# Performance work log

Hardware: AMD Instinct MI355X
Metric: run time of the kernel (lower is better)

## Reference

```python
import jax, jax.numpy as jnp
import numpy as np

B, T, C, H = 4, 1024, 768, 12
HD = C // H  # 64
EPS = 1e-5

def setup_inputs() -> dict:
    key = jax.random.key(0)
    ks = jax.random.split(key, 6)
    s = 0.02
    return {
        "x": jax.random.normal(ks[0], (B, T, C), jnp.float32),
        "ln1_w": jnp.ones((C,), jnp.float32),
        "w_attn": jax.random.normal(ks[1], (C, 3 * C), jnp.float32) * s,
        "w_pos": jax.random.normal(ks[2], (C, C), jnp.float32) * s,
        "w_cproj": jax.random.normal(ks[3], (C, C), jnp.float32) * s,
        "ln2_w": jnp.ones((C,), jnp.float32),
        "w_fc": jax.random.normal(ks[4], (C, 4 * C), jnp.float32) * s,
        "w_mproj": jax.random.normal(ks[5], (4 * C, C), jnp.float32) * s,
    }

def _layernorm(x, w):
    m = jnp.mean(x, axis=-1, keepdims=True)
    v = jnp.mean(jnp.square(x - m), axis=-1, keepdims=True)
    return (x - m) * jax.lax.rsqrt(v + EPS) * w

def _rpe_table(dtype):
    # sinusoidal table over relative distances [-(T-1), T-1] -> [2T-1, HD]
    inv_freq = 1.0 / (10000.0 ** (jnp.arange(0, HD, 2, dtype=jnp.float32) / HD))
    dist = jnp.arange(-(T - 1), T, dtype=jnp.float32)
    freqs = dist[:, None] * inv_freq[None, :]
    return jnp.concatenate([jnp.sin(freqs), jnp.cos(freqs)], axis=-1).astype(dtype)

def reference(x, ln1_w, w_attn, w_pos, w_cproj, ln2_w, w_fc, w_mproj):
    # ---- attention branch ----
    h = _layernorm(x, ln1_w)
    qkv = h @ w_attn                                 # [B,T,3C]
    q, k, v = jnp.split(qkv, 3, axis=-1)
    q = q.reshape(B, T, H, HD).transpose(0, 2, 1, 3)  # [B,H,T,HD]
    k = k.reshape(B, T, H, HD).transpose(0, 2, 1, 3)
    v = v.reshape(B, T, H, HD).transpose(0, 2, 1, 3)
    # note: the original also computes p = c_pos(x) but never uses it (dead code)

    # relative position embeddings gathered to [T,T,HD]
    idx = jnp.arange(T)
    rel = jnp.clip(idx[:, None] - idx[None, :], -(T - 1), T - 1) + (T - 1)
    rpe = _rpe_table(q.dtype)[rel]                    # [T,T,HD]

    scale = 1.0 / np.sqrt(HD)
    att = (jnp.einsum('bhid,bhjd->bhij', q, k)
           + jnp.einsum('bhid,ijd->bhij', q, rpe)) * scale
    causal = idx[:, None] >= idx[None, :]             # [T,T] lower-tri
    att = jnp.where(causal, att, -jnp.inf)
    att = jax.nn.softmax(att, axis=-1)
    y = jnp.einsum('bhij,bhjd->bhid', att, v)         # [B,H,T,HD]
    y = y.transpose(0, 2, 1, 3).reshape(B, T, C) @ w_cproj
    x = x + y

    # ---- MLP branch ----
    h2 = _layernorm(x, ln2_w)
    m = jax.nn.gelu(h2 @ w_fc, approximate=False) @ w_mproj
    return x + m
```

## Files before the change

kernel.cpp:

```cpp
#include <hip/hip_runtime.h>
#include <math.h>

typedef __attribute__((ext_vector_type(8))) short bf16x8;
typedef __attribute__((ext_vector_type(4))) float f32x4;
typedef __attribute__((ext_vector_type(16))) float f32x16;
typedef __attribute__((ext_vector_type(4))) unsigned u32x4;

__device__ inline short f2bf(float f) {
  unsigned u = __builtin_bit_cast(unsigned, f);
  u = u + 0x7fffu + ((u >> 16) & 1u);
  return (short)(u >> 16);
}
__device__ inline float bf2f(short s) {
  return __builtin_bit_cast(float, ((unsigned)(unsigned short)s) << 16);
}

__device__ inline void gload16(const short* g, short* l) {
  __builtin_amdgcn_global_load_lds(
      (const __attribute__((address_space(1))) unsigned*)g,
      (__attribute__((address_space(3))) unsigned*)l, 16, 0, 0);
}

__global__ __launch_bounds__(256) void wtrans_kernel(
    const float* __restrict__ in, short* __restrict__ out, int K, int N) {
  __shared__ float tile[32][33];
  const int tx = threadIdx.x & 31, ty = threadIdx.x >> 5;
  const int n0 = blockIdx.x * 32, k0 = blockIdx.y * 32;
  #pragma unroll
  for (int r = ty; r < 32; r += 8)
    tile[r][tx] = in[(size_t)(k0 + r) * N + n0 + tx];
  __syncthreads();
  #pragma unroll
  for (int r = ty; r < 32; r += 8)
    out[(size_t)(n0 + r) * K + k0 + tx] = f2bf(tile[tx][r]);
}

__global__ __launch_bounds__(256) void ktab_kernel(short* __restrict__ ktab) {
  const int idx = blockIdx.x * 256 + threadIdx.x;
  const int j = idx >> 5, cc = idx & 31;
  const float invf = exp2f(-(float)cc * (13.287712379549449f / 32.0f));
  const float ang = (float)j * invf;
  ktab[j * 64 + cc]      = f2bf(cosf(ang));
  ktab[j * 64 + 32 + cc] = f2bf(sinf(ang));
}

__global__ __launch_bounds__(256) void qprime_kernel(
    const short* __restrict__ qkv, short* __restrict__ qpr) {
  const int idx = blockIdx.x * 256 + threadIdx.x;
  const int cc = idx & 31;
  const int row = idx >> 5;
  const int i = row & 1023, bh = row >> 10;
  const int b = bh / 12, h = bh % 12;
  const float invf = exp2f(-(float)cc * (13.287712379549449f / 32.0f));
  const float ang = (float)i * invf;
  const float si = sinf(ang), co = cosf(ang);
  const short* q = qkv + (size_t)(b * 1024 + i) * 2304 + h * 64;
  const float qs = bf2f(q[cc]), qc = bf2f(q[32 + cc]);
  qpr[(size_t)row * 64 + cc]      = f2bf(qs * si + qc * co);
  qpr[(size_t)row * 64 + 32 + cc] = f2bf(qc * si - qs * co);
}

__global__ __launch_bounds__(256) void ln_kernel(
    const float* __restrict__ x, const float* __restrict__ w,
    short* __restrict__ out) {
  const int row = blockIdx.x, tid = threadIdx.x;
  const float* xr = x + (size_t)row * 768;
  float v0 = xr[tid], v1 = xr[tid + 256], v2 = xr[tid + 512];
  float s = v0 + v1 + v2;
  #pragma unroll
  for (int o = 1; o < 64; o <<= 1) s += __shfl_xor(s, o);
  __shared__ float red[8];
  const int wv = tid >> 6;
  if ((tid & 63) == 0) red[wv] = s;
  __syncthreads();
  const float mean = (red[0] + red[1] + red[2] + red[3]) * (1.0f / 768.0f);
  v0 -= mean; v1 -= mean; v2 -= mean;
  float q = v0 * v0 + v1 * v1 + v2 * v2;
  #pragma unroll
  for (int o = 1; o < 64; o <<= 1) q += __shfl_xor(q, o);
  if ((tid & 63) == 0) red[4 + wv] = q;
  __syncthreads();
  const float var = (red[4] + red[5] + red[6] + red[7]) * (1.0f / 768.0f);
  const float inv = 1.0f / sqrtf(var + 1e-5f);
  out[(size_t)row * 768 + tid]       = f2bf(v0 * inv * w[tid]);
  out[(size_t)row * 768 + tid + 256] = f2bf(v1 * inv * w[tid + 256]);
  out[(size_t)row * 768 + tid + 512] = f2bf(v2 * inv * w[tid + 512]);
}

__global__ __launch_bounds__(256) void vtrans_kernel(
    const short* __restrict__ qkv, short* __restrict__ vT) {
  __shared__ short tile[64][65];
  const int blk = blockIdx.x;
  const int bh = blk >> 4, t0 = (blk & 15) * 64;
  const int b = bh / 12, h = bh % 12;
  const int tx = threadIdx.x & 63, ty = threadIdx.x >> 6;
  const short* src = qkv + (size_t)(b * 1024 + t0) * 2304 + 1536 + h * 64;
  #pragma unroll
  for (int r = ty; r < 64; r += 4)
    tile[r][tx] = src[(size_t)r * 2304 + tx];
  __syncthreads();
  short* dst = vT + (size_t)bh * 64 * 1024 + t0;
  #pragma unroll
  for (int r = ty; r < 64; r += 4)
    dst[(size_t)r * 1024 + tx] = tile[tx][r];
}

template <int EPI, int BM, int BN>
__global__ __launch_bounds__(256) void gemm_bt(
    const short* __restrict__ A, const short* __restrict__ Bt,
    const float* __restrict__ res, float* __restrict__ outF,
    short* __restrict__ outB, int M, int N, int K, int lda, int ldb) {
  __shared__ __align__(16) short As[2][BM * 32];
  __shared__ __align__(16) short Bs[2][BN * 32];
  constexpr int WM = BM / 2, WN = BN / 2;
  constexpr int MI = WM / 16, NJ = WN / 16;
  const int tid = threadIdx.x;
  const int w = tid >> 6, lane = tid & 63;
  const int m0 = blockIdx.y * BM, n0 = blockIdx.x * BN;
  const int wm = (w >> 1) * WM, wn = (w & 1) * WN;
  const int lr = lane >> 2;
  const int lc = (lane & 3) * 8;
  if constexpr (EPI == 3) {
    A += (size_t)blockIdx.z * K;
    Bt += (size_t)blockIdx.z * K;
    outF += (size_t)blockIdx.z * M * N;
  }
  f32x4 acc[MI][NJ];
  #pragma unroll
  for (int i = 0; i < MI; i++)
    #pragma unroll
    for (int j = 0; j < NJ; j++)
      #pragma unroll
      for (int r = 0; r < 4; r++) acc[i][j][r] = 0.0f;

  const int nt = K / 32;
  #pragma unroll
  for (int p = 0; p < BM / 64; ++p)
    gload16(A + (size_t)(m0 + p * 64 + w * 16 + lr) * lda + lc,
            &As[0][p * 2048 + w * 512]);
  #pragma unroll
  for (int p = 0; p < BN / 64; ++p)
    gload16(Bt + (size_t)(n0 + p * 64 + w * 16 + lr) * ldb + lc,
            &Bs[0][p * 2048 + w * 512]);
  __syncthreads();

  for (int t = 0; t < nt; ++t) {
    const int cur = t & 1;
    if (t + 1 < nt) {
      const int kt = (t + 1) * 32;
      #pragma unroll
      for (int p = 0; p < BM / 64; ++p)
        gload16(A + (size_t)(m0 + p * 64 + w * 16 + lr) * lda + kt + lc,
                &As[cur ^ 1][p * 2048 + w * 512]);
      #pragma unroll
      for (int p = 0; p < BN / 64; ++p)
        gload16(Bt + (size_t)(n0 + p * 64 + w * 16 + lr) * ldb + kt + lc,
                &Bs[cur ^ 1][p * 2048 + w * 512]);
    }
    bf16x8 af[MI], bfr[NJ];
    #pragma unroll
    for (int i = 0; i < MI; i++)
      af[i] = *(const bf16x8*)&As[cur][(wm + i * 16 + (lane & 15)) * 32 + (lane >> 4) * 8];
    #pragma unroll
    for (int j = 0; j < NJ; j++)
      bfr[j] = *(const bf16x8*)&Bs[cur][(wn + j * 16 + (lane & 15)) * 32 + (lane >> 4) * 8];
    #pragma unroll
    for (int i = 0; i < MI; i++)
      #pragma unroll
      for (int j = 0; j < NJ; j++)
        acc[i][j] = __builtin_amdgcn_mfma_f32_16x16x32_bf16(af[i], bfr[j],
                                                            acc[i][j], 0, 0, 0);
    __syncthreads();
  }
  const int r0 = (lane >> 4) * 4, cl = lane & 15;
  #pragma unroll
  for (int i = 0; i < MI; i++) {
    #pragma unroll
    for (int j = 0; j < NJ; j++) {
      const int gm = m0 + wm + i * 16 + r0;
      const int gn = n0 + wn + j * 16 + cl;
      #pragma unroll
      for (int r = 0; r < 4; r++) {
        const size_t idx = (size_t)(gm + r) * N + gn;
        const float v = acc[i][j][r];
        if constexpr (EPI == 0) {
          outB[idx] = f2bf(v);
        } else if constexpr (EPI == 1) {
          outF[idx] = res[idx] + v;
        } else if constexpr (EPI == 2) {
          outB[idx] = f2bf(0.5f * v * (1.0f + erff(v * 0.70710678118f)));
        } else {
          outF[idx] = v;
        }
      }
    }
  }
}

__global__ __launch_bounds__(256) void reduce_splitk(
    const float* __restrict__ Cp, const float* __restrict__ res,
    float* __restrict__ out) {
  const size_t i4 = ((size_t)blockIdx.x * 256 + threadIdx.x) * 4;
  float4 a = *(const float4*)(res + i4);
  #pragma unroll
  for (int z = 0; z < 4; ++z) {
    float4 p = *(const float4*)(Cp + (size_t)z * 3145728 + i4);
    a.x += p.x; a.y += p.y; a.z += p.z; a.w += p.w;
  }
  *(float4*)(out + i4) = a;
}

__global__ __launch_bounds__(64) void attn_part(
    const short* __restrict__ qkv, const short* __restrict__ vT,
    const short* __restrict__ qpr, const short* __restrict__ ktab,
    float* __restrict__ mpart, float* __restrict__ lpart,
    short* __restrict__ Ypart) {
  const int blk = blockIdx.x;
  const int bh = blk / 144;
  const int rem = blk % 144;
  int g = 0;
  while (g < 7 && rem >= 2 * (g + 1) * (g + 2)) ++g;
  const int r2 = rem - 2 * g * (g + 1);
  const int it = g * 4 + r2 / (g + 1);
  const int c = r2 % (g + 1);
  const int b = bh / 12, h = bh % 12;
  const int I0 = it * 32;
  const int lane = threadIdx.x;
  const int li = lane & 31, hi = lane >> 5;

  const short* qrow = qkv + (size_t)(b * 1024 + I0 + li) * 2304 + h * 64;
  const short* qprow = qpr + ((size_t)bh * 1024 + I0 + li) * 64;
  bf16x8 qf[8];
  #pragma unroll
  for (int s = 0; s < 4; s++) {
    qf[s]     = *(const bf16x8*)(qrow + s * 16 + hi * 8);
    qf[4 + s] = *(const bf16x8*)(qprow + s * 16 + hi * 8);
  }
  const short* kbase = qkv + (size_t)(b * 1024) * 2304 + 768 + h * 64;
  const short* vbase = vT + (size_t)bh * 64 * 1024;

  float m_run = -1e30f, l_run = 0.0f;
  f32x16 ya0, ya1;
  #pragma unroll
  for (int r = 0; r < 16; r++) { ya0[r] = 0.0f; ya1[r] = 0.0f; }

  const int jt0 = c * 4;
  const int jt1 = (c * 4 + 3 < it) ? (c * 4 + 3) : it;

  bf16x8 kn[8];
  {
    const short* kb = kbase + (size_t)(jt0 * 32 + li) * 2304;
    const short* kt = ktab + (size_t)(jt0 * 32 + li) * 64;
    #pragma unroll
    for (int s = 0; s < 4; s++) {
      kn[s]     = *(const bf16x8*)(kb + s * 16 + hi * 8);
      kn[4 + s] = *(const bf16x8*)(kt + s * 16 + hi * 8);
    }
  }

  for (int jt = jt0; jt <= jt1; ++jt) {
    const int J0 = jt * 32;
    bf16x8 kf[8];
    #pragma unroll
    for (int s = 0; s < 8; s++) kf[s] = kn[s];
    if (jt < jt1) {
      const short* kb = kbase + (size_t)((jt + 1) * 32 + li) * 2304;
      const short* kt = ktab + (size_t)((jt + 1) * 32 + li) * 64;
      #pragma unroll
      for (int s = 0; s < 4; s++) {
        kn[s]     = *(const bf16x8*)(kb + s * 16 + hi * 8);
        kn[4 + s] = *(const bf16x8*)(kt + s * 16 + hi * 8);
      }
    }
    bf16x8 vc[4];
    #pragma unroll
    for (int s = 0; s < 2; s++) {
      vc[s * 2]     = *(const bf16x8*)(vbase + (size_t)li * 1024 + J0 + s * 16 + hi * 8);
      vc[s * 2 + 1] = *(const bf16x8*)(vbase + (size_t)(32 + li) * 1024 + J0 + s * 16 + hi * 8);
    }
    f32x16 sa0, sa1;
    #pragma unroll
    for (int r = 0; r < 16; r++) { sa0[r] = 0.0f; sa1[r] = 0.0f; }
    #pragma unroll
    for (int s = 0; s < 4; s++) {
      sa0 = __builtin_amdgcn_mfma_f32_32x32x16_bf16(kf[2 * s],     qf[2 * s],     sa0, 0, 0, 0);
      sa1 = __builtin_amdgcn_mfma_f32_32x32x16_bf16(kf[2 * s + 1], qf[2 * s + 1], sa1, 0, 0, 0);
    }
    const int gi = I0 + li;
    float sv[16];
    float mx = -1e30f;
    #pragma unroll
    for (int r = 0; r < 16; r++) {
      const int j = (r & 3) + 8 * (r >> 2) + 4 * hi;
      float v = (sa0[r] + sa1[r]) * 0.125f;
      v = (J0 + j <= gi) ? v : -1e30f;
      sv[r] = v;
      mx = fmaxf(mx, v);
    }
    mx = fmaxf(mx, __shfl_xor(mx, 32));
    float mref = m_run;
    float alpha = 1.0f;
    const bool resc = !__all(mx <= m_run + 8.0f);
    if (resc) {
      mref = fmaxf(m_run, mx);
      alpha = __expf(m_run - mref);
      m_run = mref;
    }
    float psum = 0.0f;
    unsigned pw[8];
    #pragma unroll
    for (int t = 0; t < 8; t++) {
      const float p0 = __expf(sv[2 * t] - mref);
      const float p1 = __expf(sv[2 * t + 1] - mref);
      psum += p0 + p1;
      pw[t] = (unsigned)(unsigned short)f2bf(p0) |
              ((unsigned)(unsigned short)f2bf(p1) << 16);
    }
    psum += __shfl_xor(psum, 32);
    l_run = l_run * alpha + psum;
    if (resc) {
      #pragma unroll
      for (int r = 0; r < 16; r++) {
        const int row = (r & 3) + 8 * (r >> 2) + 4 * hi;
        const float a = __shfl(alpha, row);
        ya0[r] *= a;
        ya1[r] *= a;
      }
    }
    #pragma unroll
    for (int s = 0; s < 2; s++) {
      unsigned a0 = pw[4 * s],     b0 = pw[4 * s + 2];
      unsigned a1 = pw[4 * s + 1], b1 = pw[4 * s + 3];
      asm volatile("v_permlane32_swap_b32 %0, %1" : "+v"(a0), "+v"(b0));
      asm volatile("v_permlane32_swap_b32 %0, %1" : "+v"(a1), "+v"(b1));
      u32x4 t4;
      t4[0] = a0; t4[1] = a1; t4[2] = b0; t4[3] = b1;
      const bf16x8 pf = __builtin_bit_cast(bf16x8, t4);
      ya0 = __builtin_amdgcn_mfma_f32_32x32x16_bf16(pf, vc[s * 2],     ya0, 0, 0, 0);
      ya1 = __builtin_amdgcn_mfma_f32_32x32x16_bf16(pf, vc[s * 2 + 1], ya1, 0, 0, 0);
    }
  }
  if (hi == 0) {
    mpart[(size_t)blk * 32 + li] = m_run;
    lpart[(size_t)blk * 32 + li] = l_run;
  }
  short* yb = Ypart + (size_t)blk * 2048;
  #pragma unroll
  for (int r = 0; r < 16; r++) {
    const int row = (r & 3) + 8 * (r >> 2) + 4 * hi;
    yb[row * 64 + li]      = f2bf(ya0[r]);
    yb[row * 64 + 32 + li] = f2bf(ya1[r]);
  }
}

__global__ __launch_bounds__(256) void attn_combine(
    const float* __restrict__ mpart, const float* __restrict__ lpart,
    const short* __restrict__ Ypart, short* __restrict__ yout) {
  const int blk = blockIdx.x;
  const int it = blk & 31, bh = blk >> 5;
  const int b = bh / 12, h = bh % 12;
  const int g = it >> 2;
  const int nc = g + 1;
  const int base = bh * 144 + 2 * g * (g + 1) + (it - g * 4) * (g + 1);
  const int row = threadIdx.x >> 3;
  const int c0 = (threadIdx.x & 7) * 8;
  float mv[8], lv[8], wgt[8];
  float m = -1e30f;
  #pragma unroll
  for (int cI = 0; cI < 8; ++cI) {
    mv[cI] = (cI < nc) ? mpart[(size_t)(base + cI) * 32 + row] : -1e30f;
    lv[cI] = (cI < nc) ? lpart[(size_t)(base + cI) * 32 + row] : 0.0f;
    m = fmaxf(m, mv[cI]);
  }
  float L = 0.0f;
  #pragma unroll
  for (int cI = 0; cI < 8; ++cI) {
    wgt[cI] = __expf(mv[cI] - m);
    L += lv[cI] * wgt[cI];
  }
  const float inv = 1.0f / L;
  float y[8];
  #pragma unroll
  for (int r = 0; r < 8; r++) y[r] = 0.0f;
  #pragma unroll
  for (int cI = 0; cI < 8; ++cI) {
    if (cI < nc) {
      bf16x8 v = *(const bf16x8*)(Ypart + ((size_t)(base + cI) * 32 + row) * 64 + c0);
      #pragma unroll
      for (int r = 0; r < 8; r++) y[r] += bf2f(v[r]) * wgt[cI];
    }
  }
  short* dst = yout + (size_t)(b * 1024 + it * 32 + row) * 768 + h * 64 + c0;
  #pragma unroll
  for (int r = 0; r < 8; r++) dst[r] = f2bf(y[r] * inv);
}

extern "C" void kernel_launch(void* const* d_in, const int* in_sizes, int n_in,
                              void* d_out, int out_size, void* d_ws, size_t ws_size,
                              hipStream_t stream) {
  const float* x       = (const float*)d_in[0];
  const float* ln1_w   = (const float*)d_in[1];
  const float* w_attn  = (const float*)d_in[2];
  const float* w_cproj = (const float*)d_in[4];
  const float* ln2_w   = (const float*)d_in[5];
  const float* w_fc    = (const float*)d_in[6];
  const float* w_mproj = (const float*)d_in[7];
  float* out = (float*)d_out;
  char* ws = (char*)d_ws;

  short* wT_attn  = (short*)(ws + 0);
  short* wT_cproj = (short*)(ws + 3538944);
  short* wT_fc    = (short*)(ws + 4718592);
  short* wT_mproj = (short*)(ws + 9437184);
  short* ktab     = (short*)(ws + 14155776);
  short* h_bf     = (short*)(ws + 14417920);
  short* qpr      = (short*)(ws + 14417920);
  short* qkv_bf   = (short*)(ws + 20709376);
  short* vT       = (short*)(ws + 39583744);
  short* y_att    = (short*)(ws + 45875200);
  short* h2_bf    = (short*)(ws + 52166656);
  short* hfc_bf   = (short*)(ws + 58458112);
  float* mpart = (float*)(ws + 52166656);
  float* lpart = (float*)(ws + 53051392);
  short* Ypart = (short*)(ws + 53936128);
  float* Cpart = (float*)(ws + 83623936);
  const bool use_splitk = ws_size >= 133955584ull;

  wtrans_kernel<<<dim3(72, 24), 256, 0, stream>>>(w_attn, wT_attn, 768, 2304);
  wtrans_kernel<<<dim3(24, 24), 256, 0, stream>>>(w_cproj, wT_cproj, 768, 768);
  wtrans_kernel<<<dim3(96, 24), 256, 0, stream>>>(w_fc, wT_fc, 768, 3072);
  wtrans_kernel<<<dim3(24, 96), 256, 0, stream>>>(w_mproj, wT_mproj, 3072, 768);
  ktab_kernel<<<128, 256, 0, stream>>>(ktab);

  ln_kernel<<<4096, 256, 0, stream>>>(x, ln1_w, h_bf);
  gemm_bt<0, 128, 128><<<dim3(18, 32), 256, 0, stream>>>(
      h_bf, wT_attn, nullptr, nullptr, qkv_bf, 4096, 2304, 768, 768, 768);
  qprime_kernel<<<6144, 256, 0, stream>>>(qkv_bf, qpr);
  vtrans_kernel<<<768, 256, 0, stream>>>(qkv_bf, vT);
  attn_part<<<6912, 64, 0, stream>>>(qkv_bf, vT, qpr, ktab, mpart, lpart, Ypart);
  attn_combine<<<1536, 256, 0, stream>>>(mpart, lpart, Ypart, y_att);
  gemm_bt<1, 64, 64><<<dim3(12, 64), 256, 0, stream>>>(
      y_att, wT_cproj, x, out, nullptr, 4096, 768, 768, 768, 768);
  ln_kernel<<<4096, 256, 0, stream>>>(out, ln2_w, h2_bf);
  gemm_bt<2, 128, 128><<<dim3(24, 32), 256, 0, stream>>>(
      h2_bf, wT_fc, nullptr, nullptr, hfc_bf, 4096, 3072, 768, 768, 768);
  if (use_splitk) {
    gemm_bt<3, 128, 128><<<dim3(6, 32, 4), 256, 0, stream>>>(
        hfc_bf, wT_mproj, nullptr, Cpart, nullptr, 4096, 768, 768, 3072, 3072);
    reduce_splitk<<<3072, 256, 0, stream>>>(Cpart, out, out);
  } else {
    gemm_bt<1, 64, 64><<<dim3(12, 64), 256, 0, stream>>>(
        hfc_bf, wT_mproj, out, out, nullptr, 4096, 768, 3072, 3072, 3072);
  }
}
```

Measured before the change: 230.7 us.

## Fuse split-KV attention partials and combine into one block with LDS reduction

The separate attention partial kernel and combine kernel become one kernel. Each block of 8 waves handles one 32-row query tile, with each wave covering one KV chunk, and partial results are merged in shared memory instead of going through global m/l/Y buffers. The four weight-transpose launches are merged into one, the ktab generation is folded into qprime (which now uses __sincosf), and softmax moves to the exp2 domain with a packed bf16 conversion and a causal mask applied only on the diagonal tile. This removes launches and global round-trips, at the cost of idle waves in early row tiles, which lowers occupancy and gives uneven per-block work.

```diff
diff --git a/kernel.cpp b/kernel.cpp
--- a/kernel.cpp
+++ b/kernel.cpp
@@ -14,6 +14,11 @@
 __device__ inline float bf2f(short s) {
   return __builtin_bit_cast(float, ((unsigned)(unsigned short)s) << 16);
 }
+__device__ inline unsigned cvt_pk_bf16(float lo, float hi) {
+  unsigned r;
+  asm("v_cvt_pk_bf16_f32 %0, %1, %2" : "=v"(r) : "v"(lo), "v"(hi));
+  return r;
+}
 
 __device__ inline void gload16(const short* g, short* l) {
   __builtin_amdgcn_global_load_lds(
@@ -21,11 +26,20 @@
       (__attribute__((address_space(3))) unsigned*)l, 16, 0, 0);
 }
 
-__global__ __launch_bounds__(256) void wtrans_kernel(
-    const float* __restrict__ in, short* __restrict__ out, int K, int N) {
+__global__ __launch_bounds__(256) void wtrans_all(
+    const float* __restrict__ wa, const float* __restrict__ wc,
+    const float* __restrict__ wf, const float* __restrict__ wm,
+    short* __restrict__ oa, short* __restrict__ oc,
+    short* __restrict__ of, short* __restrict__ om) {
   __shared__ float tile[32][33];
+  int blk = blockIdx.x;
+  const float* in; short* out; int K, N, bx;
+  if (blk < 1728)      { in = wa; out = oa; K = 768;  N = 2304; bx = 72; }
+  else if (blk < 2304) { blk -= 1728; in = wc; out = oc; K = 768;  N = 768;  bx = 24; }
+  else if (blk < 4608) { blk -= 2304; in = wf; out = of; K = 768;  N = 3072; bx = 96; }
+  else                 { blk -= 4608; in = wm; out = om; K = 3072; N = 768;  bx = 24; }
+  const int n0 = (blk % bx) * 32, k0 = (blk / bx) * 32;
   const int tx = threadIdx.x & 31, ty = threadIdx.x >> 5;
-  const int n0 = blockIdx.x * 32, k0 = blockIdx.y * 32;
   #pragma unroll
   for (int r = ty; r < 32; r += 8)
     tile[r][tx] = in[(size_t)(k0 + r) * N + n0 + tx];
@@ -35,17 +49,9 @@
     out[(size_t)(n0 + r) * K + k0 + tx] = f2bf(tile[tx][r]);
 }
 
-__global__ __launch_bounds__(256) void ktab_kernel(short* __restrict__ ktab) {
-  const int idx = blockIdx.x * 256 + threadIdx.x;
-  const int j = idx >> 5, cc = idx & 31;
-  const float invf = exp2f(-(float)cc * (13.287712379549449f / 32.0f));
-  const float ang = (float)j * invf;
-  ktab[j * 64 + cc]      = f2bf(cosf(ang));
-  ktab[j * 64 + 32 + cc] = f2bf(sinf(ang));
-}
-
 __global__ __launch_bounds__(256) void qprime_kernel(
-    const short* __restrict__ qkv, short* __restrict__ qpr) {
+    const short* __restrict__ qkv, short* __restrict__ qpr,
+    short* __restrict__ ktab) {
   const int idx = blockIdx.x * 256 + threadIdx.x;
   const int cc = idx & 31;
   const int row = idx >> 5;
@@ -53,7 +59,12 @@
   const int b = bh / 12, h = bh % 12;
   const float invf = exp2f(-(float)cc * (13.287712379549449f / 32.0f));
   const float ang = (float)i * invf;
-  const float si = sinf(ang), co = cosf(ang);
+  float si, co;
+  __sincosf(ang, &si, &co);
+  if (bh == 0) {
+    ktab[i * 64 + cc]      = f2bf(co);
+    ktab[i * 64 + 32 + cc] = f2bf(si);
+  }
   const short* q = qkv + (size_t)(b * 1024 + i) * 2304 + h * 64;
   const float qs = bf2f(q[cc]), qc = bf2f(q[32 + cc]);
   qpr[(size_t)row * 64 + cc]      = f2bf(qs * si + qc * co);
@@ -210,189 +221,172 @@
   *(float4*)(out + i4) = a;
 }
 
-__global__ __launch_bounds__(64) void attn_part(
+__global__ __launch_bounds__(512) void attn_fused(
     const short* __restrict__ qkv, const short* __restrict__ vT,
     const short* __restrict__ qpr, const short* __restrict__ ktab,
-    float* __restrict__ mpart, float* __restrict__ lpart,
-    short* __restrict__ Ypart) {
+    short* __restrict__ yout) {
+  __shared__ float Ylds[8][32][64];
+  __shared__ float Mlds[8][32], Llds[8][32];
   const int blk = blockIdx.x;
-  const int bh = blk / 144;
-  const int rem = blk % 144;
-  int g = 0;
-  while (g < 7 && rem >= 2 * (g + 1) * (g + 2)) ++g;
-  const int r2 = rem - 2 * g * (g + 1);
-  const int it = g * 4 + r2 / (g + 1);
-  const int c = r2 % (g + 1);
+  const int it = blk & 31, bh = blk >> 5;
   const int b = bh / 12, h = bh % 12;
   const int I0 = it * 32;
-  const int lane = threadIdx.x;
+  const int tid = threadIdx.x;
+  const int w = tid >> 6;
+  const int lane = tid & 63;
   const int li = lane & 31, hi = lane >> 5;
-
-  const short* qrow = qkv + (size_t)(b * 1024 + I0 + li) * 2304 + h * 64;
-  const short* qprow = qpr + ((size_t)bh * 1024 + I0 + li) * 64;
-  bf16x8 qf[8];
-  #pragma unroll
-  for (int s = 0; s < 4; s++) {
-    qf[s]     = *(const bf16x8*)(qrow + s * 16 + hi * 8);
-    qf[4 + s] = *(const bf16x8*)(qprow + s * 16 + hi * 8);
-  }
-  const short* kbase = qkv + (size_t)(b * 1024) * 2304 + 768 + h * 64;
-  const short* vbase = vT + (size_t)bh * 64 * 1024;
-
-  float m_run = -1e30f, l_run = 0.0f;
-  f32x16 ya0, ya1;
-  #pragma unroll
-  for (int r = 0; r < 16; r++) { ya0[r] = 0.0f; ya1[r] = 0.0f; }
-
-  const int jt0 = c * 4;
-  const int jt1 = (c * 4 + 3 < it) ? (c * 4 + 3) : it;
-
-  bf16x8 kn[8];
-  {
-    const short* kb = kbase + (size_t)(jt0 * 32 + li) * 2304;
-    const short* kt = ktab + (size_t)(jt0 * 32 + li) * 64;
+  const int g = it >> 2;
+  const bool active = (w <= g);
+  constexpr float SCALE2 = 0.125f * 1.44269504089f;
+
+  if (active) {
+    const short* qrow = qkv + (size_t)(b * 1024 + I0 + li) * 2304 + h * 64;
+    const short* qprow = qpr + ((size_t)bh * 1024 + I0 + li) * 64;
+    bf16x8 qf[8];
     #pragma unroll
     for (int s = 0; s < 4; s++) {
-      kn[s]     = *(const bf16x8*)(kb + s * 16 + hi * 8);
-      kn[4 + s] = *(const bf16x8*)(kt + s * 16 + hi * 8);
-    }
-  }
-
-  for (int jt = jt0; jt <= jt1; ++jt) {
-    const int J0 = jt * 32;
-    bf16x8 kf[8];
-    #pragma unroll
-    for (int s = 0; s < 8; s++) kf[s] = kn[s];
-    if (jt < jt1) {
-      const short* kb = kbase + (size_t)((jt + 1) * 32 + li) * 2304;
-      const short* kt = ktab + (size_t)((jt + 1) * 32 + li) * 64;
+      qf[s]     = *(const bf16x8*)(qrow + s * 16 + hi * 8);
+      qf[4 + s] = *(const bf16x8*)(qprow + s * 16 + hi * 8);
+    }
+    const short* kbase = qkv + (size_t)(b * 1024) * 2304 + 768 + h * 64;
+    const short* vbase = vT + (size_t)bh * 64 * 1024;
+
+    float m_run = -1e30f, l_run = 0.0f;
+    f32x16 ya0, ya1;
+    #pragma unroll
+    for (int r = 0; r < 16; r++) { ya0[r] = 0.0f; ya1[r] = 0.0f; }
+
+    const int jt0 = w * 4;
+    const int jt1 = (w * 4 + 3 < it) ? (w * 4 + 3) : it;
+
+    bf16x8 kn[8];
+    {
+      const short* kb = kbase + (size_t)(jt0 * 32 + li) * 2304;
+      const short* kt = ktab + (size_t)(jt0 * 32 + li) * 64;
       #pragma unroll
       for (int s = 0; s < 4; s++) {
         kn[s]     = *(const bf16x8*)(kb + s * 16 + hi * 8);
         kn[4 + s] = *(const bf16x8*)(kt + s * 16 + hi * 8);
       }
     }
-    bf16x8 vc[4];
-    #pragma unroll
-    for (int s = 0; s < 2; s++) {
-      vc[s * 2]     = *(const bf16x8*)(vbase + (size_t)li * 1024 + J0 + s * 16 + hi * 8);
-      vc[s * 2 + 1] = *(const bf16x8*)(vbase + (size_t)(32 + li) * 1024 + J0 + s * 16 + hi * 8);
-    }
-    f32x16 sa0, sa1;
-    #pragma unroll
-    for (int r = 0; r < 16; r++) { sa0[r] = 0.0f; sa1[r] = 0.0f; }
-    #pragma unroll
-    for (int s = 0; s < 4; s++) {
-      sa0 = __builtin_amdgcn_mfma_f32_32x32x16_bf16(kf[2 * s],     qf[2 * s],     sa0, 0, 0, 0);
-      sa1 = __builtin_amdgcn_mfma_f32_32x32x16_bf16(kf[2 * s + 1], qf[2 * s + 1], sa1, 0, 0, 0);
-    }
-    const int gi = I0 + li;
-    float sv[16];
-    float mx = -1e30f;
+
+    for (int jt = jt0; jt <= jt1; ++jt) {
+      const int J0 = jt * 32;
+      bf16x8 kf[8];
+      #pragma unroll
+      for (int s = 0; s < 8; s++) kf[s] = kn[s];
+      if (jt < jt1) {
+        const short* kb = kbase + (size_t)((jt + 1) * 32 + li) * 2304;
+        const short* kt = ktab + (size_t)((jt + 1) * 32 + li) * 64;
+        #pragma unroll
+        for (int s = 0; s < 4; s++) {
+          kn[s]     = *(const bf16x8*)(kb + s * 16 + hi * 8);
+          kn[4 + s] = *(const bf16x8*)(kt + s * 16 + hi * 8);
+        }
+      }
+      bf16x8 vc[4];
+      #pragma unroll
+      for (int s = 0; s < 2; s++) {
+        vc[s * 2]     = *(const bf16x8*)(vbase + (size_t)li * 1024 + J0 + s * 16 + hi * 8);
+        vc[s * 2 + 1] = *(const bf16x8*)(vbase + (size_t)(32 + li) * 1024 + J0 + s * 16 + hi * 8);
+      }
+      f32x16 sa0, sa1;
+      #pragma unroll
+      for (int r = 0; r < 16; r++) { sa0[r] = 0.0f; sa1[r] = 0.0f; }
+      #pragma unroll
+      for (int s = 0; s < 4; s++) {
+        sa0 = __builtin_amdgcn_mfma_f32_32x32x16_bf16(kf[2 * s],     qf[2 * s],     sa0, 0, 0, 0);
+        sa1 = __builtin_amdgcn_mfma_f32_32x32x16_bf16(kf[2 * s + 1], qf[2 * s + 1], sa1, 0, 0, 0);
+      }
+      float sv[16];
+      float mx = -1e30f;
+      if (jt == it) {
+        #pragma unroll
+        for (int r = 0; r < 16; r++) {
+          const int j = (r & 3) + 8 * (r >> 2) + 4 * hi;
+          float v = (sa0[r] + sa1[r]) * SCALE2;
+          v = (j <= li) ? v : -1e30f;
+          sv[r] = v;
+          mx = fmaxf(mx, v);
+        }
+      } else {
+        #pragma unroll
+        for (int r = 0; r < 16; r++) {
+          const float v = (sa0[r] + sa1[r]) * SCALE2;
+          sv[r] = v;
+          mx = fmaxf(mx, v);
+        }
+      }
+      mx = fmaxf(mx, __shfl_xor(mx, 32));
+      float mref = m_run;
+      float alpha = 1.0f;
+      const bool resc = !__all(mx <= m_run + 11.5f);
+      if (resc) {
+        mref = fmaxf(m_run, mx);
+        alpha = exp2f(m_run - mref);
+        m_run = mref;
+      }
+      float psum = 0.0f;
+      unsigned pw[8];
+      #pragma unroll
+      for (int t = 0; t < 8; t++) {
+        const float p0 = exp2f(sv[2 * t] - mref);
+        const float p1 = exp2f(sv[2 * t + 1] - mref);
+        psum += p0 + p1;
+        pw[t] = cvt_pk_bf16(p0, p1);
+      }
+      psum += __shfl_xor(psum, 32);
+      l_run = l_run * alpha + psum;
+      if (resc) {
+        #pragma unroll
+        for (int r = 0; r < 16; r++) {
+          const int row = (r & 3) + 8 * (r >> 2) + 4 * hi;
+          const float a = __shfl(alpha, row);
+          ya0[r] *= a;
+          ya1[r] *= a;
+        }
+      }
+      #pragma unroll
+      for (int s = 0; s < 2; s++) {
+        unsigned a0 = pw[4 * s],     b0 = pw[4 * s + 2];
+        unsigned a1 = pw[4 * s + 1], b1 = pw[4 * s + 3];
+        asm volatile("v_permlane32_swap_b32 %0, %1" : "+v"(a0), "+v"(b0));
+        asm volatile("v_permlane32_swap_b32 %0, %1" : "+v"(a1), "+v"(b1));
+        u32x4 t4;
+        t4[0] = a0; t4[1] = a1; t4[2] = b0; t4[3] = b1;
+        const bf16x8 pf = __builtin_bit_cast(bf16x8, t4);
+        ya0 = __builtin_amdgcn_mfma_f32_32x32x16_bf16(pf, vc[s * 2],     ya0, 0, 0, 0);
+        ya1 = __builtin_amdgcn_mfma_f32_32x32x16_bf16(pf, vc[s * 2 + 1], ya1, 0, 0, 0);
+      }
+    }
+    if (hi == 0) {
+      Mlds[w][li] = m_run;
+      Llds[w][li] = l_run;
+    }
     #pragma unroll
     for (int r = 0; r < 16; r++) {
-      const int j = (r & 3) + 8 * (r >> 2) + 4 * hi;
-      float v = (sa0[r] + sa1[r]) * 0.125f;
-      v = (J0 + j <= gi) ? v : -1e30f;
-      sv[r] = v;
-      mx = fmaxf(mx, v);
-    }
-    mx = fmaxf(mx, __shfl_xor(mx, 32));
-    float mref = m_run;
-    float alpha = 1.0f;
-    const bool resc = !__all(mx <= m_run + 8.0f);
-    if (resc) {
-      mref = fmaxf(m_run, mx);
-      alpha = __expf(m_run - mref);
-      m_run = mref;
-    }
-    float psum = 0.0f;
-    unsigned pw[8];
-    #pragma unroll
-    for (int t = 0; t < 8; t++) {
-      const float p0 = __expf(sv[2 * t] - mref);
-      const float p1 = __expf(sv[2 * t + 1] - mref);
-      psum += p0 + p1;
-      pw[t] = (unsigned)(unsigned short)f2bf(p0) |
-              ((unsigned)(unsigned short)f2bf(p1) << 16);
-    }
-    psum += __shfl_xor(psum, 32);
-    l_run = l_run * alpha + psum;
-    if (resc) {
-      #pragma unroll
-      for (int r = 0; r < 16; r++) {
-        const int row = (r & 3) + 8 * (r >> 2) + 4 * hi;
-        const float a = __shfl(alpha, row);
-        ya0[r] *= a;
-        ya1[r] *= a;
-      }
-    }
-    #pragma unroll
-    for (int s = 0; s < 2; s++) {
-      unsigned a0 = pw[4 * s],     b0 = pw[4 * s + 2];
-      unsigned a1 = pw[4 * s + 1], b1 = pw[4 * s + 3];
-      asm volatile("v_permlane32_swap_b32 %0, %1" : "+v"(a0), "+v"(b0));
-      asm volatile("v_permlane32_swap_b32 %0, %1" : "+v"(a1), "+v"(b1));
-      u32x4 t4;
-      t4[0] = a0; t4[1] = a1; t4[2] = b0; t4[3] = b1;
-      const bf16x8 pf = __builtin_bit_cast(bf16x8, t4);
-      ya0 = __builtin_amdgcn_mfma_f32_32x32x16_bf16(pf, vc[s * 2],     ya0, 0, 0, 0);
-      ya1 = __builtin_amdgcn_mfma_f32_32x32x16_bf16(pf, vc[s * 2 + 1], ya1, 0, 0, 0);
-    }
-  }
-  if (hi == 0) {
-    mpart[(size_t)blk * 32 + li] = m_run;
-    lpart[(size_t)blk * 32 + li] = l_run;
-  }
-  short* yb = Ypart + (size_t)blk * 2048;
-  #pragma unroll
-  for (int r = 0; r < 16; r++) {
-    const int row = (r & 3) + 8 * (r >> 2) + 4 * hi;
-    yb[row * 64 + li]      = f2bf(ya0[r]);
-    yb[row * 64 + 32 + li] = f2bf(ya1[r]);
-  }
-}
-
-__global__ __launch_bounds__(256) void attn_combine(
-    const float* __restrict__ mpart, const float* __restrict__ lpart,
-    const short* __restrict__ Ypart, short* __restrict__ yout) {
-  const int blk = blockIdx.x;
-  const int it = blk & 31, bh = blk >> 5;
-  const int b = bh / 12, h = bh % 12;
-  const int g = it >> 2;
-  const int nc = g + 1;
-  const int base = bh * 144 + 2 * g * (g + 1) + (it - g * 4) * (g + 1);
-  const int row = threadIdx.x >> 3;
-  const int c0 = (threadIdx.x & 7) * 8;
-  float mv[8], lv[8], wgt[8];
+      const int row = (r & 3) + 8 * (r >> 2) + 4 * hi;
+      Ylds[w][row][li]      = ya0[r];
+      Ylds[w][row][32 + li] = ya1[r];
+    }
+  }
+  __syncthreads();
+  const int row = tid >> 4;
+  const int c4 = (tid & 15) * 4;
   float m = -1e30f;
-  #pragma unroll
-  for (int cI = 0; cI < 8; ++cI) {
-    mv[cI] = (cI < nc) ? mpart[(size_t)(base + cI) * 32 + row] : -1e30f;
-    lv[cI] = (cI < nc) ? lpart[(size_t)(base + cI) * 32 + row] : 0.0f;
-    m = fmaxf(m, mv[cI]);
-  }
-  float L = 0.0f;
-  #pragma unroll
-  for (int cI = 0; cI < 8; ++cI) {
-    wgt[cI] = __expf(mv[cI] - m);
-    L += lv[cI] * wgt[cI];
+  for (int cI = 0; cI <= g; ++cI) m = fmaxf(m, Mlds[cI][row]);
+  float L = 0.0f, y0 = 0.0f, y1 = 0.0f, y2 = 0.0f, y3 = 0.0f;
+  for (int cI = 0; cI <= g; ++cI) {
+    const float wgt = exp2f(Mlds[cI][row] - m);
+    L += Llds[cI][row] * wgt;
+    const float* yr = &Ylds[cI][row][c4];
+    y0 += yr[0] * wgt; y1 += yr[1] * wgt; y2 += yr[2] * wgt; y3 += yr[3] * wgt;
   }
   const float inv = 1.0f / L;
-  float y[8];
-  #pragma unroll
-  for (int r = 0; r < 8; r++) y[r] = 0.0f;
-  #pragma unroll
-  for (int cI = 0; cI < 8; ++cI) {
-    if (cI < nc) {
-      bf16x8 v = *(const bf16x8*)(Ypart + ((size_t)(base + cI) * 32 + row) * 64 + c0);
-      #pragma unroll
-      for (int r = 0; r < 8; r++) y[r] += bf2f(v[r]) * wgt[cI];
-    }
-  }
-  short* dst = yout + (size_t)(b * 1024 + it * 32 + row) * 768 + h * 64 + c0;
-  #pragma unroll
-  for (int r = 0; r < 8; r++) dst[r] = f2bf(y[r] * inv);
+  uint2 o;
+  o.x = cvt_pk_bf16(y0 * inv, y1 * inv);
+  o.y = cvt_pk_bf16(y2 * inv, y3 * inv);
+  *(uint2*)(yout + (size_t)(b * 1024 + I0 + row) * 768 + h * 64 + c4) = o;
 }
 
 extern "C" void kernel_launch(void* const* d_in, const int* in_sizes, int n_in,
@@ -420,25 +414,18 @@
   short* y_att    = (short*)(ws + 45875200);
   short* h2_bf    = (short*)(ws + 52166656);
   short* hfc_bf   = (short*)(ws + 58458112);
-  float* mpart = (float*)(ws + 52166656);
-  float* lpart = (float*)(ws + 53051392);
-  short* Ypart = (short*)(ws + 53936128);
   float* Cpart = (float*)(ws + 83623936);
   const bool use_splitk = ws_size >= 133955584ull;
 
-  wtrans_kernel<<<dim3(72, 24), 256, 0, stream>>>(w_attn, wT_attn, 768, 2304);
-  wtrans_kernel<<<dim3(24, 24), 256, 0, stream>>>(w_cproj, wT_cproj, 768, 768);
-  wtrans_kernel<<<dim3(96, 24), 256, 0, stream>>>(w_fc, wT_fc, 768, 3072);
-  wtrans_kernel<<<dim3(24, 96), 256, 0, stream>>>(w_mproj, wT_mproj, 3072, 768);
-  ktab_kernel<<<128, 256, 0, stream>>>(ktab);
+  wtrans_all<<<6912, 256, 0, stream>>>(w_attn, w_cproj, w_fc, w_mproj,
+                                       wT_attn, wT_cproj, wT_fc, wT_mproj);
 
   ln_kernel<<<4096, 256, 0, stream>>>(x, ln1_w, h_bf);
   gemm_bt<0, 128, 128><<<dim3(18, 32), 256, 0, stream>>>(
       h_bf, wT_attn, nullptr, nullptr, qkv_bf, 4096, 2304, 768, 768, 768);
-  qprime_kernel<<<6144, 256, 0, stream>>>(qkv_bf, qpr);
+  qprime_kernel<<<6144, 256, 0, stream>>>(qkv_bf, qpr, ktab);
   vtrans_kernel<<<768, 256, 0, stream>>>(qkv_bf, vT);
-  attn_part<<<6912, 64, 0, stream>>>(qkv_bf, vT, qpr, ktab, mpart, lpart, Ypart);
-  attn_combine<<<1536, 256, 0, stream>>>(mpart, lpart, Ypart, y_att);
+  attn_fused<<<1536, 512, 0, stream>>>(qkv_bf, vT, qpr, ktab, y_att);
   gemm_bt<1, 64, 64><<<dim3(12, 64), 256, 0, stream>>>(
       y_att, wT_cproj, x, out, nullptr, 4096, 768, 768, 768, 768);
   ln_kernel<<<4096, 256, 0, stream>>>(out, ln2_w, h2_bf);
```

Measured after the change: 250.3 us. 1.09x slower.
